# Performance work log

Hardware: AMD Instinct MI355X
Metric: run time of the kernel (lower is better)

## Reference

```python
import jax, jax.numpy as jnp
import numpy as np
from jax import lax

EPS = 1e-07
PATCH = 3  # patch_size -> padding = 1 with 1x1 kernels
PROP = 3   # propagate_size -> 3x3 sum pool (avg_pool*9)


def setup_inputs() -> dict:
    key = jax.random.key(0)
    k1, k2 = jax.random.split(key)
    foreground = jax.random.normal(k1, (4, 128, 64, 64), dtype=jnp.float32)
    mask = jax.random.uniform(k2, (4, 1, 64, 64), dtype=jnp.float32)
    return {"foreground": foreground, "mask": mask}


def _cattention_single(x, m):
    # x: (c, h, w); m: (1, h, w)
    c, h, w = x.shape
    pad = PATCH // 2  # = 1
    # dynamic 1x1 conv kernels: (h*w, c), one kernel per spatial location
    k = x.reshape(c, h * w).T + EPS
    k = k / jnp.sqrt(jnp.sum(k * k, axis=1, keepdims=True))
    # F.conv2d(x, k, padding=1) with 1x1 kernels -> zero-pad then matmul
    x_pad = jnp.pad(x, ((0, 0), (pad, pad), (pad, pad)))  # (c, h+2, w+2)
    scores = jnp.einsum('lc,cij->lij', k, x_pad)  # (hw, h+2, w+2)
    # avg_pool2d(3,1,padding=1) * 9 == 3x3 sum pool with zero padding
    scores = lax.reduce_window(scores, 0.0, lax.add,
                               window_dimensions=(1, 3, 3),
                               window_strides=(1, 1, 1),
                               padding=((0, 0), (1, 1), (1, 1)))
    att = jax.nn.softmax(scores, axis=0)  # softmax over the hw channel dim
    # conv_transpose2d with 1x1 kernels, padding=1 -> crop border then matmul
    att_c = att[:, pad:-pad, pad:-pad]  # (hw, h, w)
    recovered = jnp.einsum('lij,lc->cij', att_c, k)  # (c, h, w)
    recovered = recovered * (1.0 - m) / float(PATCH ** 2)
    return recovered + x * m


def reference(foreground, mask):
    return jax.vmap(_cattention_single)(foreground, mask)
```

## Files before the change

kernel.cpp:

```cpp
#include <hip/hip_runtime.h>


typedef short bf16x8 __attribute__((ext_vector_type(8)));
typedef float f32x4 __attribute__((ext_vector_type(4)));

#define L2E 1.4426950408889634f

__device__ __forceinline__ unsigned short f2bf(float f) {
    unsigned int u;
    __builtin_memcpy(&u, &f, 4);
    u = u + 0x7FFFu + ((u >> 16) & 1u);
    return (unsigned short)(u >> 16);
}

__global__ void prep_k(const float* __restrict__ x,
                       unsigned short* __restrict__ kmat,
                       unsigned short* __restrict__ kT) {
    const int b = blockIdx.y, l0 = blockIdx.x * 64, t = threadIdx.x;
    const int wave = t >> 6, lane = t & 63;
    const float* xb = x + (size_t)b * 128 * 4096;
    __shared__ float sqp[256];
    __shared__ __align__(16) unsigned short sT[64 * 136];

    float xv[32];
    float sq = 0.f;
#pragma unroll
    for (int i = 0; i < 32; i++) {
        int c = wave * 32 + i;
        float v = xb[(size_t)c * 4096 + l0 + lane] + 1e-7f;
        xv[i] = v;
        sq += v * v;
    }
    sqp[t] = sq;
    __syncthreads();
    const float inv = rsqrtf(sqp[lane] + sqp[64 + lane] + sqp[128 + lane] + sqp[192 + lane]);

    unsigned int* sT32 = (unsigned int*)sT;
#pragma unroll
    for (int i = 0; i < 16; i++) {
        int c = wave * 32 + i * 2;
        unsigned int pack = (unsigned int)f2bf(xv[2 * i] * inv) |
                            ((unsigned int)f2bf(xv[2 * i + 1] * inv) << 16);
        sT32[(lane * 136 + c) >> 1] = pack;
    }
    __syncthreads();
#pragma unroll
    for (int i = 0; i < 4; i++) {
        int e = i * 2048 + t * 8, row = e >> 7, col = e & 127;
        *(bf16x8*)(kmat + ((size_t)b * 4096 + l0 + row) * 128 + col) =
            *(const bf16x8*)(sT + row * 136 + col);
    }
    unsigned short* ktb = kT + (size_t)b * 128 * 4096;
#pragma unroll
    for (int i = 0; i < 32; i++) {
        int c = wave * 32 + i;
        ktb[(size_t)c * 4096 + l0 + lane] = sT[lane * 136 + c];
    }
}

__global__ void prep_xb(const float* __restrict__ x,
                        unsigned short* __restrict__ xbT) {
    const int b = blockIdx.y, p = blockIdx.x, t = threadIdx.x;
    __shared__ float sX[8][3][66];
    __shared__ __align__(16) unsigned short sQ[64 * 136];

    for (int c0 = 0; c0 < 128; c0 += 8) {
        __syncthreads();
#pragma unroll
        for (int i = 0; i < 6; i++) {
            int j = t + i * 256;
            int cc = j / 192, rem = j % 192;
            int r = rem >> 6, q = rem & 63;
            int pp = p + r - 1;
            float v = 0.f;
            if ((unsigned)pp < 64u)
                v = x[((size_t)b * 128 + c0 + cc) * 4096 + pp * 64 + q];
            sX[cc][r][1 + q] = v;
        }
        if (t < 48) {
            int cc = t / 6, r = (t % 6) >> 1, side = t & 1;
            sX[cc][r][side * 65] = 0.f;
        }
        __syncthreads();
#pragma unroll
        for (int h = 0; h < 2; h++) {
            int idx = t + h * 256;
            int cc = idx >> 6, q = idx & 63;
            float s = 0.f;
#pragma unroll
            for (int r = 0; r < 3; r++)
                s += sX[cc][r][q] + sX[cc][r][q + 1] + sX[cc][r][q + 2];
            sQ[q * 136 + c0 + cc] = f2bf(s * L2E);
        }
    }
    __syncthreads();
#pragma unroll
    for (int i = 0; i < 4; i++) {
        int e = i * 2048 + t * 8, row = e >> 7, col = e & 127;
        *(bf16x8*)(xbT + ((size_t)b * 4096 + p * 64 + row) * 128 + col) =
            *(const bf16x8*)(sQ + row * 136 + col);
    }
}

#define SK_STRIDE 136
#define SV_STRIDE 72
#define SP_STRIDE 72
#define SK_ELEMS (64 * SK_STRIDE)
#define SV_ELEMS (128 * SV_STRIDE)
#define SP_ELEMS (4 * 32 * SP_STRIDE)
#define SMEM_ELEMS (SK_ELEMS + SV_ELEMS + SP_ELEMS)

__global__ void __launch_bounds__(256, 2) flash_attn(
        const unsigned short* __restrict__ kmat,
        const unsigned short* __restrict__ kT,
        const unsigned short* __restrict__ xbT,
        float* __restrict__ opart,
        float* __restrict__ lsum,
        int nsplit) {
    const int combo = blockIdx.x & (4 * nsplit - 1);
    const int qb = blockIdx.x / (4 * nsplit);
    const int b = combo & 3, split = combo >> 2;
    const int nk = 4096 / nsplit, kt_base = split * nk, NIT = nk >> 6;
    const int t = threadIdx.x;
    const int wave = t >> 6, lane = t & 63;
    const int l16 = lane & 15, quad = lane >> 4;

    __shared__ __align__(16) unsigned short smem[SMEM_ELEMS];
    unsigned short* sK = smem;
    unsigned short* sV = smem + SK_ELEMS;
    unsigned short* sP = smem + SK_ELEMS + SV_ELEMS + wave * 32 * SP_STRIDE;

    bf16x8 aq[2][4];
#pragma unroll
    for (int h = 0; h < 2; h++) {
        const unsigned short* xq =
            xbT + ((size_t)b * 4096 + qb * 128 + wave * 32 + h * 16 + l16) * 128 + quad * 8;
#pragma unroll
        for (int cc = 0; cc < 4; cc++) aq[h][cc] = *(const bf16x8*)(xq + cc * 32);
    }

    f32x4 o[2][8];
#pragma unroll
    for (int h = 0; h < 2; h++)
#pragma unroll
        for (int n = 0; n < 8; n++) o[h][n] = (f32x4){0.f, 0.f, 0.f, 0.f};
    float rs[2][4] = {{0.f, 0.f, 0.f, 0.f}, {0.f, 0.f, 0.f, 0.f}};

    const unsigned short* kmb = kmat + (size_t)b * 4096 * 128;
    const unsigned short* ktb = kT + (size_t)b * 128 * 4096;

    bf16x8 kreg[4], vreg[4];
#pragma unroll
    for (int i = 0; i < 4; i++) {
        int e = i * 2048 + t * 8;
        kreg[i] = *(const bf16x8*)(kmb + (size_t)(kt_base + (e >> 7)) * 128 + (e & 127));
        vreg[i] = *(const bf16x8*)(ktb + (size_t)(e >> 6) * 4096 + kt_base + (e & 63));
    }

    for (int it = 0; it < NIT; it++) {
        __syncthreads();
#pragma unroll
        for (int i = 0; i < 4; i++) {
            int e = i * 2048 + t * 8;
            *(bf16x8*)(sK + (e >> 7) * SK_STRIDE + (e & 127)) = kreg[i];
            *(bf16x8*)(sV + (e >> 6) * SV_STRIDE + (e & 63)) = vreg[i];
        }
        __syncthreads();
        if (it + 1 < NIT) {
            const int kt0 = kt_base + (it + 1) * 64;
#pragma unroll
            for (int i = 0; i < 4; i++) {
                int e = i * 2048 + t * 8;
                kreg[i] = *(const bf16x8*)(kmb + (size_t)(kt0 + (e >> 7)) * 128 + (e & 127));
                vreg[i] = *(const bf16x8*)(ktb + (size_t)(e >> 6) * 4096 + kt0 + (e & 63));
            }
        }

        f32x4 s[2][4];
#pragma unroll
        for (int h = 0; h < 2; h++)
#pragma unroll
            for (int k4 = 0; k4 < 4; k4++) s[h][k4] = (f32x4){0.f, 0.f, 0.f, 0.f};
#pragma unroll
        for (int cc = 0; cc < 4; cc++) {
#pragma unroll
            for (int k4 = 0; k4 < 4; k4++) {
                bf16x8 bf = *(const bf16x8*)(sK + (k4 * 16 + l16) * SK_STRIDE + cc * 32 + quad * 8);
#pragma unroll
                for (int h = 0; h < 2; h++)
                    s[h][k4] = __builtin_amdgcn_mfma_f32_16x16x32_bf16(aq[h][cc], bf, s[h][k4], 0, 0, 0);
            }
        }

#pragma unroll
        for (int h = 0; h < 2; h++)
#pragma unroll
            for (int k4 = 0; k4 < 4; k4++)
#pragma unroll
                for (int r = 0; r < 4; r++) {
                    float p = exp2f(s[h][k4][r]);
                    s[h][k4][r] = p;
                    rs[h][r] += p;
                }

#pragma unroll
        for (int h = 0; h < 2; h++)
#pragma unroll
            for (int k4 = 0; k4 < 4; k4++)
#pragma unroll
                for (int r = 0; r < 4; r++)
                    sP[(h * 16 + quad * 4 + r) * SP_STRIDE + k4 * 16 + l16] = f2bf(s[h][k4][r]);
        asm volatile("" ::: "memory");
        __threadfence_block();
        bf16x8 pa[2][2];
#pragma unroll
        for (int h = 0; h < 2; h++)
#pragma unroll
            for (int kc = 0; kc < 2; kc++)
                pa[h][kc] = *(const bf16x8*)(sP + (h * 16 + l16) * SP_STRIDE + kc * 32 + quad * 8);
        asm volatile("" ::: "memory");

#pragma unroll
        for (int kc = 0; kc < 2; kc++)
#pragma unroll
            for (int n = 0; n < 8; n++) {
                bf16x8 bf = *(const bf16x8*)(sV + (n * 16 + l16) * SV_STRIDE + kc * 32 + quad * 8);
#pragma unroll
                for (int h = 0; h < 2; h++)
                    o[h][n] = __builtin_amdgcn_mfma_f32_16x16x32_bf16(pa[h][kc], bf, o[h][n], 0, 0, 0);
            }
    }

#pragma unroll
    for (int off = 1; off < 16; off <<= 1)
#pragma unroll
        for (int h = 0; h < 2; h++)
#pragma unroll
            for (int r = 0; r < 4; r++) rs[h][r] += __shfl_xor(rs[h][r], off);
    if (l16 == 0) {
#pragma unroll
        for (int h = 0; h < 2; h++)
#pragma unroll
            for (int r = 0; r < 4; r++) {
                int q = qb * 128 + wave * 32 + h * 16 + quad * 4 + r;
                lsum[(size_t)(split * 4 + b) * 4096 + q] = rs[h][r];
            }
    }

    float* sO = reinterpret_cast<float*>(smem);
#pragma unroll
    for (int half = 0; half < 2; half++) {
        __syncthreads();
        if ((wave >> 1) == half) {
#pragma unroll
            for (int h = 0; h < 2; h++)
#pragma unroll
                for (int n = 0; n < 8; n++)
#pragma unroll
                    for (int r = 0; r < 4; r++)
                        sO[(n * 16 + l16) * 68 + (wave & 1) * 32 + h * 16 + quad * 4 + r] =
                            o[h][n][r];
        }
        __syncthreads();
#pragma unroll
        for (int i = 0; i < 8; i++) {
            int c = (t >> 4) + i * 16, qj = (t & 15) * 4;
            *(f32x4*)(opart + ((size_t)(split * 4 + b) * 128 + c) * 4096 +
                      qb * 128 + half * 64 + qj) = *(const f32x4*)(sO + c * 68 + qj);
        }
    }
}

__global__ void combine(const float* __restrict__ opart,
                        const float* __restrict__ lsum,
                        const float* __restrict__ x,
                        const float* __restrict__ mask,
                        float* __restrict__ out, int S) {
    const int b = blockIdx.y, qb = blockIdx.x, t = threadIdx.x;
    __shared__ float Linv[64];
    if (t < 64) {
        int q = qb * 64 + t;
        float L = 0.f;
        for (int s = 0; s < S; s++) L += lsum[(size_t)(s * 4 + b) * 4096 + q];
        Linv[t] = 1.f / fmaxf(L, 1e-37f);
    }
    __syncthreads();
#pragma unroll
    for (int i = 0; i < 8; i++) {
        int c = (t >> 4) + i * 16, qj = (t & 15) * 4;
        size_t qoff = (size_t)qb * 64 + qj;
        f32x4 acc = (f32x4){0.f, 0.f, 0.f, 0.f};
        for (int s = 0; s < S; s++) {
            f32x4 p = *(const f32x4*)(opart + ((size_t)(s * 4 + b) * 128 + c) * 4096 + qoff);
#pragma unroll
            for (int j = 0; j < 4; j++) acc[j] += p[j];
        }
        f32x4 xv = *(const f32x4*)(x + ((size_t)b * 128 + c) * 4096 + qoff);
        f32x4 mv = *(const f32x4*)(mask + (size_t)b * 4096 + qoff);
        f32x4 res;
#pragma unroll
        for (int j = 0; j < 4; j++)
            res[j] = acc[j] * Linv[qj + j] * (1.f - mv[j]) * (1.f / 9.f) + xv[j] * mv[j];
        *(f32x4*)(out + ((size_t)b * 128 + c) * 4096 + qoff) = res;
    }
}

extern "C" void kernel_launch(void* const* d_in, const int* in_sizes, int n_in,
                              void* d_out, int out_size, void* d_ws, size_t ws_size,
                              hipStream_t stream) {
    const float* x = (const float*)d_in[0];
    const float* mask = (const float*)d_in[1];
    float* out = (float*)d_out;
    char* ws = (char*)d_ws;
    unsigned short* kmat = (unsigned short*)(ws);
    unsigned short* kT   = (unsigned short*)(ws + (size_t)4 * 1024 * 1024);
    unsigned short* xbT  = (unsigned short*)(ws + (size_t)8 * 1024 * 1024);
    float* lsum  = (float*)(ws + (size_t)12 * 1024 * 1024);
    float* opart = (float*)(ws + (size_t)12 * 1024 * 1024 + 512 * 1024);

    int S;
    if (ws_size >= (size_t)46661632) S = 4;
    else if (ws_size >= (size_t)29884416) S = 2;
    else if (ws_size >= (size_t)21495808) S = 1;
    else return;

    prep_k<<<dim3(64, 4), 256, 0, stream>>>(x, kmat, kT);
    prep_xb<<<dim3(64, 4), 256, 0, stream>>>(x, xbT);
    flash_attn<<<dim3(32 * 4 * S), 256, 0, stream>>>(kmat, kT, xbT, opart, lsum, S);
    combine<<<dim3(64, 4), 256, 0, stream>>>(opart, lsum, x, mask, out, S);
}
```

Measured before the change: 168.3 us.

## Fuse prep kernels, fold combine into attention via atomic last-block reduction

Merges the two prep kernels into one that computes normalized K, K transpose and the box-summed query in a single pass over x. The attention kernel now reads K fragments straight from global memory instead of staging them in LDS, stores partial outputs as bf16, and doubles the key split count with higher occupancy. The separate combine kernel is removed: the last split block per tile, detected with an atomic counter, does the reduction, normalization and mask blend. This cuts launches and traffic, but adds bf16 rounding of the partial outputs and a dependence on correct counter reset and memory fences.

```diff
diff --git a/kernel.cpp b/kernel.cpp
--- a/kernel.cpp
+++ b/kernel.cpp
@@ -3,6 +3,8 @@
 
 typedef short bf16x8 __attribute__((ext_vector_type(8)));
 typedef float f32x4 __attribute__((ext_vector_type(4)));
+typedef unsigned short u16x4 __attribute__((ext_vector_type(4)));
+typedef unsigned int u32x2 __attribute__((ext_vector_type(2)));
 
 #define L2E 1.4426950408889634f
 
@@ -12,123 +14,133 @@
     u = u + 0x7FFFu + ((u >> 16) & 1u);
     return (unsigned short)(u >> 16);
 }
-
-__global__ void prep_k(const float* __restrict__ x,
-                       unsigned short* __restrict__ kmat,
-                       unsigned short* __restrict__ kT) {
-    const int b = blockIdx.y, l0 = blockIdx.x * 64, t = threadIdx.x;
-    const int wave = t >> 6, lane = t & 63;
-    const float* xb = x + (size_t)b * 128 * 4096;
+__device__ __forceinline__ float bf2f(unsigned short h) {
+    unsigned int u = ((unsigned int)h) << 16;
+    float f;
+    __builtin_memcpy(&f, &u, 4);
+    return f;
+}
+__device__ __forceinline__ unsigned int pk_bf16(float a, float b) {
+    unsigned int ua, ub;
+    __builtin_memcpy(&ua, &a, 4);
+    __builtin_memcpy(&ub, &b, 4);
+    return ((ua + 0x8000u) >> 16) | ((ub + 0x8000u) & 0xFFFF0000u);
+}
+
+__global__ void prep(const float* __restrict__ x,
+                     unsigned short* __restrict__ kmat,
+                     unsigned short* __restrict__ kT,
+                     unsigned short* __restrict__ xbT,
+                     unsigned int* __restrict__ counters) {
+    const int p = blockIdx.x, qh = blockIdx.y, b = blockIdx.z, t = threadIdx.x;
+    const int q0 = qh * 32;
+    if (qh == 0 && t == 0) counters[b * 32 + (p >> 1)] = 0;
+
+    __shared__ float sX[8][3][36];
+    __shared__ float sMidT[32 * 132];
+    __shared__ __align__(16) unsigned short sQ[32 * 136];
     __shared__ float sqp[256];
-    __shared__ __align__(16) unsigned short sT[64 * 136];
-
-    float xv[32];
-    float sq = 0.f;
-#pragma unroll
-    for (int i = 0; i < 32; i++) {
-        int c = wave * 32 + i;
-        float v = xb[(size_t)c * 4096 + l0 + lane] + 1e-7f;
-        xv[i] = v;
-        sq += v * v;
-    }
-    sqp[t] = sq;
+    __shared__ float sInv[32];
+
+    const int ccOwn = t >> 5, qOwn = t & 31;
+    float sqacc = 0.f;
+
+    for (int c0 = 0; c0 < 128; c0 += 8) {
+        __syncthreads();
+#pragma unroll
+        for (int i = 0; i < 4; i++) {
+            int j = i * 256 + t;
+            if (j < 816) {
+                int cc = j / 102, rem = j - cc * 102;
+                int r = rem / 34, qq = rem - r * 34;
+                int pp = p + r - 1, qg = q0 + qq - 1;
+                float v = 0.f;
+                if ((unsigned)pp < 64u && (unsigned)qg < 64u)
+                    v = x[((size_t)b * 128 + c0 + cc) * 4096 + pp * 64 + qg];
+                sX[cc][r][qq] = v;
+            }
+        }
+        __syncthreads();
+        float mid = sX[ccOwn][1][qOwn + 1] + 1e-7f;
+        sMidT[qOwn * 132 + c0 + ccOwn] = mid;
+        sqacc += mid * mid;
+        float sbox = 0.f;
+#pragma unroll
+        for (int r = 0; r < 3; r++)
+            sbox += sX[ccOwn][r][qOwn] + sX[ccOwn][r][qOwn + 1] + sX[ccOwn][r][qOwn + 2];
+        sQ[qOwn * 136 + c0 + ccOwn] = f2bf(sbox * L2E);
+    }
+    sqp[ccOwn * 32 + qOwn] = sqacc;
     __syncthreads();
-    const float inv = rsqrtf(sqp[lane] + sqp[64 + lane] + sqp[128 + lane] + sqp[192 + lane]);
-
-    unsigned int* sT32 = (unsigned int*)sT;
-#pragma unroll
-    for (int i = 0; i < 16; i++) {
-        int c = wave * 32 + i * 2;
-        unsigned int pack = (unsigned int)f2bf(xv[2 * i] * inv) |
-                            ((unsigned int)f2bf(xv[2 * i + 1] * inv) << 16);
-        sT32[(lane * 136 + c) >> 1] = pack;
+    if (t < 32) {
+        float ss = 0.f;
+#pragma unroll
+        for (int g = 0; g < 8; g++) ss += sqp[g * 32 + t];
+        sInv[t] = rsqrtf(ss);
     }
     __syncthreads();
-#pragma unroll
-    for (int i = 0; i < 4; i++) {
-        int e = i * 2048 + t * 8, row = e >> 7, col = e & 127;
-        *(bf16x8*)(kmat + ((size_t)b * 4096 + l0 + row) * 128 + col) =
-            *(const bf16x8*)(sT + row * 136 + col);
-    }
-    unsigned short* ktb = kT + (size_t)b * 128 * 4096;
-#pragma unroll
-    for (int i = 0; i < 32; i++) {
-        int c = wave * 32 + i;
-        ktb[(size_t)c * 4096 + l0 + lane] = sT[lane * 136 + c];
-    }
-}
-
-__global__ void prep_xb(const float* __restrict__ x,
-                        unsigned short* __restrict__ xbT) {
-    const int b = blockIdx.y, p = blockIdx.x, t = threadIdx.x;
-    __shared__ float sX[8][3][66];
-    __shared__ __align__(16) unsigned short sQ[64 * 136];
-
-    for (int c0 = 0; c0 < 128; c0 += 8) {
-        __syncthreads();
-#pragma unroll
-        for (int i = 0; i < 6; i++) {
-            int j = t + i * 256;
-            int cc = j / 192, rem = j % 192;
-            int r = rem >> 6, q = rem & 63;
-            int pp = p + r - 1;
-            float v = 0.f;
-            if ((unsigned)pp < 64u)
-                v = x[((size_t)b * 128 + c0 + cc) * 4096 + pp * 64 + q];
-            sX[cc][r][1 + q] = v;
-        }
-        if (t < 48) {
-            int cc = t / 6, r = (t % 6) >> 1, side = t & 1;
-            sX[cc][r][side * 65] = 0.f;
-        }
-        __syncthreads();
-#pragma unroll
-        for (int h = 0; h < 2; h++) {
-            int idx = t + h * 256;
-            int cc = idx >> 6, q = idx & 63;
-            float s = 0.f;
-#pragma unroll
-            for (int r = 0; r < 3; r++)
-                s += sX[cc][r][q] + sX[cc][r][q + 1] + sX[cc][r][q + 2];
-            sQ[q * 136 + c0 + cc] = f2bf(s * L2E);
-        }
-    }
-    __syncthreads();
-#pragma unroll
-    for (int i = 0; i < 4; i++) {
-        int e = i * 2048 + t * 8, row = e >> 7, col = e & 127;
-        *(bf16x8*)(xbT + ((size_t)b * 4096 + p * 64 + row) * 128 + col) =
+
+#pragma unroll
+    for (int i = 0; i < 2; i++) {
+        int e = (i * 256 + t) * 8, row = e >> 7, col = e & 127;
+        *(bf16x8*)(xbT + ((size_t)b * 4096 + p * 64 + q0 + row) * 128 + col) =
             *(const bf16x8*)(sQ + row * 136 + col);
     }
-}
-
-#define SK_STRIDE 136
+#pragma unroll
+    for (int i = 0; i < 2; i++) {
+        int u = i * 256 + t, q = u >> 4, cg = u & 15;
+        float iv = sInv[q];
+        f32x4 a = *(const f32x4*)(sMidT + q * 132 + cg * 8);
+        f32x4 c = *(const f32x4*)(sMidT + q * 132 + cg * 8 + 4);
+        unsigned int w[4];
+        w[0] = pk_bf16(a[0] * iv, a[1] * iv);
+        w[1] = pk_bf16(a[2] * iv, a[3] * iv);
+        w[2] = pk_bf16(c[0] * iv, c[1] * iv);
+        w[3] = pk_bf16(c[2] * iv, c[3] * iv);
+        *(uint4*)(kmat + ((size_t)b * 4096 + p * 64 + q0 + q) * 128 + cg * 8) =
+            make_uint4(w[0], w[1], w[2], w[3]);
+    }
+    {
+        int c = t >> 1, half = t & 1;
+        unsigned int w[8];
+#pragma unroll
+        for (int j = 0; j < 8; j++) {
+            int ql = half * 16 + j * 2;
+            w[j] = pk_bf16(sMidT[ql * 132 + c] * sInv[ql],
+                           sMidT[(ql + 1) * 132 + c] * sInv[ql + 1]);
+        }
+        unsigned short* dst = kT + ((size_t)b * 128 + c) * 4096 + p * 64 + q0 + half * 16;
+        *(uint4*)(dst) = make_uint4(w[0], w[1], w[2], w[3]);
+        *(uint4*)(dst + 8) = make_uint4(w[4], w[5], w[6], w[7]);
+    }
+}
+
 #define SV_STRIDE 72
-#define SP_STRIDE 72
-#define SK_ELEMS (64 * SK_STRIDE)
-#define SV_ELEMS (128 * SV_STRIDE)
-#define SP_ELEMS (4 * 32 * SP_STRIDE)
-#define SMEM_ELEMS (SK_ELEMS + SV_ELEMS + SP_ELEMS)
-
-__global__ void __launch_bounds__(256, 2) flash_attn(
+
+__global__ void __launch_bounds__(256, 3) flash_attn(
         const unsigned short* __restrict__ kmat,
         const unsigned short* __restrict__ kT,
         const unsigned short* __restrict__ xbT,
-        float* __restrict__ opart,
+        const float* __restrict__ x,
+        const float* __restrict__ mask,
+        unsigned short* __restrict__ opart,
         float* __restrict__ lsum,
-        int nsplit) {
+        float* __restrict__ out,
+        unsigned int* __restrict__ counters,
+        int nsplit, int qbshift) {
     const int combo = blockIdx.x & (4 * nsplit - 1);
-    const int qb = blockIdx.x / (4 * nsplit);
+    const int qb = blockIdx.x >> qbshift;
     const int b = combo & 3, split = combo >> 2;
-    const int nk = 4096 / nsplit, kt_base = split * nk, NIT = nk >> 6;
+    const int nk = 4096 / nsplit, NIT = nk >> 6, kt_base = split * nk;
     const int t = threadIdx.x;
     const int wave = t >> 6, lane = t & 63;
     const int l16 = lane & 15, quad = lane >> 4;
 
-    __shared__ __align__(16) unsigned short smem[SMEM_ELEMS];
-    unsigned short* sK = smem;
-    unsigned short* sV = smem + SK_ELEMS;
-    unsigned short* sP = smem + SK_ELEMS + SV_ELEMS + wave * 32 * SP_STRIDE;
+    __shared__ __align__(16) unsigned short smem[18432];
+    unsigned short* sV = smem;
+    unsigned short* sP = smem + 9216 + wave * 2304;
+    __shared__ float Linv[128];
+    __shared__ int isLast;
 
     bf16x8 aq[2][4];
 #pragma unroll
@@ -144,16 +156,16 @@
     for (int h = 0; h < 2; h++)
 #pragma unroll
         for (int n = 0; n < 8; n++) o[h][n] = (f32x4){0.f, 0.f, 0.f, 0.f};
-    float rs[2][4] = {{0.f, 0.f, 0.f, 0.f}, {0.f, 0.f, 0.f, 0.f}};
+    float rs[2] = {0.f, 0.f};
 
     const unsigned short* kmb = kmat + (size_t)b * 4096 * 128;
     const unsigned short* ktb = kT + (size_t)b * 128 * 4096;
-
-    bf16x8 kreg[4], vreg[4];
+    const unsigned short* kf = kmb + (size_t)(kt_base + l16) * 128 + quad * 8;
+
+    bf16x8 vreg[4];
 #pragma unroll
     for (int i = 0; i < 4; i++) {
         int e = i * 2048 + t * 8;
-        kreg[i] = *(const bf16x8*)(kmb + (size_t)(kt_base + (e >> 7)) * 128 + (e & 127));
         vreg[i] = *(const bf16x8*)(ktb + (size_t)(e >> 6) * 4096 + kt_base + (e & 63));
     }
 
@@ -162,16 +174,14 @@
 #pragma unroll
         for (int i = 0; i < 4; i++) {
             int e = i * 2048 + t * 8;
-            *(bf16x8*)(sK + (e >> 7) * SK_STRIDE + (e & 127)) = kreg[i];
             *(bf16x8*)(sV + (e >> 6) * SV_STRIDE + (e & 63)) = vreg[i];
         }
         __syncthreads();
         if (it + 1 < NIT) {
-            const int kt0 = kt_base + (it + 1) * 64;
+            int kt0 = kt_base + (it + 1) * 64;
 #pragma unroll
             for (int i = 0; i < 4; i++) {
                 int e = i * 2048 + t * 8;
-                kreg[i] = *(const bf16x8*)(kmb + (size_t)(kt0 + (e >> 7)) * 128 + (e & 127));
                 vreg[i] = *(const bf16x8*)(ktb + (size_t)(e >> 6) * 4096 + kt0 + (e & 63));
             }
         }
@@ -181,70 +191,58 @@
         for (int h = 0; h < 2; h++)
 #pragma unroll
             for (int k4 = 0; k4 < 4; k4++) s[h][k4] = (f32x4){0.f, 0.f, 0.f, 0.f};
+        const unsigned short* kfi = kf + (size_t)it * 64 * 128;
 #pragma unroll
         for (int cc = 0; cc < 4; cc++) {
 #pragma unroll
             for (int k4 = 0; k4 < 4; k4++) {
-                bf16x8 bf = *(const bf16x8*)(sK + (k4 * 16 + l16) * SK_STRIDE + cc * 32 + quad * 8);
-#pragma unroll
-                for (int h = 0; h < 2; h++)
-                    s[h][k4] = __builtin_amdgcn_mfma_f32_16x16x32_bf16(aq[h][cc], bf, s[h][k4], 0, 0, 0);
-            }
-        }
-
+                bf16x8 kfr = *(const bf16x8*)(kfi + k4 * 2048 + cc * 32);
+                s[0][k4] = __builtin_amdgcn_mfma_f32_16x16x32_bf16(kfr, aq[0][cc], s[0][k4], 0, 0, 0);
+                s[1][k4] = __builtin_amdgcn_mfma_f32_16x16x32_bf16(kfr, aq[1][cc], s[1][k4], 0, 0, 0);
+            }
+        }
+
+#pragma unroll
+        for (int h = 0; h < 2; h++) {
+#pragma unroll
+            for (int k4 = 0; k4 < 4; k4++) {
+                float p0 = exp2f(s[h][k4][0]), p1 = exp2f(s[h][k4][1]);
+                float p2 = exp2f(s[h][k4][2]), p3 = exp2f(s[h][k4][3]);
+                rs[h] += (p0 + p1) + (p2 + p3);
+                u32x2 d;
+                d[0] = pk_bf16(p0, p1);
+                d[1] = pk_bf16(p2, p3);
+                *(u32x2*)(sP + (h * 16 + l16) * 72 + k4 * 16 + quad * 4) = d;
+            }
+        }
+        asm volatile("" ::: "memory");
+        bf16x8 pa[2][2];
 #pragma unroll
         for (int h = 0; h < 2; h++)
 #pragma unroll
-            for (int k4 = 0; k4 < 4; k4++)
-#pragma unroll
-                for (int r = 0; r < 4; r++) {
-                    float p = exp2f(s[h][k4][r]);
-                    s[h][k4][r] = p;
-                    rs[h][r] += p;
-                }
-
+            for (int kc = 0; kc < 2; kc++)
+                pa[h][kc] = *(const bf16x8*)(sP + (h * 16 + l16) * 72 + kc * 32 + quad * 8);
+        asm volatile("" ::: "memory");
+
+#pragma unroll
+        for (int kc = 0; kc < 2; kc++)
+#pragma unroll
+            for (int n = 0; n < 8; n++) {
+                bf16x8 bv = *(const bf16x8*)(sV + (n * 16 + l16) * SV_STRIDE + kc * 32 + quad * 8);
+                o[0][n] = __builtin_amdgcn_mfma_f32_16x16x32_bf16(pa[0][kc], bv, o[0][n], 0, 0, 0);
+                o[1][n] = __builtin_amdgcn_mfma_f32_16x16x32_bf16(pa[1][kc], bv, o[1][n], 0, 0, 0);
+            }
+    }
+
+#pragma unroll
+    for (int h = 0; h < 2; h++) {
+        rs[h] += __shfl_xor(rs[h], 16);
+        rs[h] += __shfl_xor(rs[h], 32);
+    }
+    if (lane < 16) {
 #pragma unroll
         for (int h = 0; h < 2; h++)
-#pragma unroll
-            for (int k4 = 0; k4 < 4; k4++)
-#pragma unroll
-                for (int r = 0; r < 4; r++)
-                    sP[(h * 16 + quad * 4 + r) * SP_STRIDE + k4 * 16 + l16] = f2bf(s[h][k4][r]);
-        asm volatile("" ::: "memory");
-        __threadfence_block();
-        bf16x8 pa[2][2];
-#pragma unroll
-        for (int h = 0; h < 2; h++)
-#pragma unroll
-            for (int kc = 0; kc < 2; kc++)
-                pa[h][kc] = *(const bf16x8*)(sP + (h * 16 + l16) * SP_STRIDE + kc * 32 + quad * 8);
-        asm volatile("" ::: "memory");
-
-#pragma unroll
-        for (int kc = 0; kc < 2; kc++)
-#pragma unroll
-            for (int n = 0; n < 8; n++) {
-                bf16x8 bf = *(const bf16x8*)(sV + (n * 16 + l16) * SV_STRIDE + kc * 32 + quad * 8);
-#pragma unroll
-                for (int h = 0; h < 2; h++)
-                    o[h][n] = __builtin_amdgcn_mfma_f32_16x16x32_bf16(pa[h][kc], bf, o[h][n], 0, 0, 0);
-            }
-    }
-
-#pragma unroll
-    for (int off = 1; off < 16; off <<= 1)
-#pragma unroll
-        for (int h = 0; h < 2; h++)
-#pragma unroll
-            for (int r = 0; r < 4; r++) rs[h][r] += __shfl_xor(rs[h][r], off);
-    if (l16 == 0) {
-#pragma unroll
-        for (int h = 0; h < 2; h++)
-#pragma unroll
-            for (int r = 0; r < 4; r++) {
-                int q = qb * 128 + wave * 32 + h * 16 + quad * 4 + r;
-                lsum[(size_t)(split * 4 + b) * 4096 + q] = rs[h][r];
-            }
+            lsum[(size_t)(split * 4 + b) * 4096 + qb * 128 + wave * 32 + h * 16 + lane] = rs[h];
     }
 
     float* sO = reinterpret_cast<float*>(smem);
@@ -263,45 +261,50 @@
         }
         __syncthreads();
 #pragma unroll
-        for (int i = 0; i < 8; i++) {
-            int c = (t >> 4) + i * 16, qj = (t & 15) * 4;
-            *(f32x4*)(opart + ((size_t)(split * 4 + b) * 128 + c) * 4096 +
-                      qb * 128 + half * 64 + qj) = *(const f32x4*)(sO + c * 68 + qj);
-        }
-    }
-}
-
-__global__ void combine(const float* __restrict__ opart,
-                        const float* __restrict__ lsum,
-                        const float* __restrict__ x,
-                        const float* __restrict__ mask,
-                        float* __restrict__ out, int S) {
-    const int b = blockIdx.y, qb = blockIdx.x, t = threadIdx.x;
-    __shared__ float Linv[64];
-    if (t < 64) {
-        int q = qb * 64 + t;
+        for (int i = 0; i < 4; i++) {
+            int u = i * 256 + t, c = u >> 3, g = u & 7;
+            f32x4 v0 = *(const f32x4*)(sO + c * 68 + g * 8);
+            f32x4 v1 = *(const f32x4*)(sO + c * 68 + g * 8 + 4);
+            unsigned int w[4];
+            w[0] = pk_bf16(v0[0], v0[1]);
+            w[1] = pk_bf16(v0[2], v0[3]);
+            w[2] = pk_bf16(v1[0], v1[1]);
+            w[3] = pk_bf16(v1[2], v1[3]);
+            *(uint4*)(opart + ((size_t)(split * 4 + b) * 128 + c) * 4096 +
+                      qb * 128 + half * 64 + g * 8) = make_uint4(w[0], w[1], w[2], w[3]);
+        }
+    }
+
+    __threadfence();
+    if (t == 0)
+        isLast = (atomicAdd(&counters[b * 32 + qb], 1u) == (unsigned)(nsplit - 1));
+    __syncthreads();
+    if (!isLast) return;
+    __threadfence();
+    if (t < 128) {
         float L = 0.f;
-        for (int s = 0; s < S; s++) L += lsum[(size_t)(s * 4 + b) * 4096 + q];
+        for (int s2 = 0; s2 < nsplit; s2++)
+            L += lsum[(size_t)(s2 * 4 + b) * 4096 + qb * 128 + t];
         Linv[t] = 1.f / fmaxf(L, 1e-37f);
     }
     __syncthreads();
-#pragma unroll
-    for (int i = 0; i < 8; i++) {
-        int c = (t >> 4) + i * 16, qj = (t & 15) * 4;
-        size_t qoff = (size_t)qb * 64 + qj;
+#pragma unroll 4
+    for (int i = 0; i < 16; i++) {
+        int u = i * 256 + t, c = u >> 5, qg = u & 31, q0 = qg * 4;
         f32x4 acc = (f32x4){0.f, 0.f, 0.f, 0.f};
-        for (int s = 0; s < S; s++) {
-            f32x4 p = *(const f32x4*)(opart + ((size_t)(s * 4 + b) * 128 + c) * 4096 + qoff);
-#pragma unroll
-            for (int j = 0; j < 4; j++) acc[j] += p[j];
-        }
-        f32x4 xv = *(const f32x4*)(x + ((size_t)b * 128 + c) * 4096 + qoff);
-        f32x4 mv = *(const f32x4*)(mask + (size_t)b * 4096 + qoff);
+        for (int s2 = 0; s2 < nsplit; s2++) {
+            u16x4 pv = *(const u16x4*)(opart + ((size_t)(s2 * 4 + b) * 128 + c) * 4096 +
+                                       qb * 128 + q0);
+#pragma unroll
+            for (int j = 0; j < 4; j++) acc[j] += bf2f(pv[j]);
+        }
+        f32x4 xv = *(const f32x4*)(x + ((size_t)b * 128 + c) * 4096 + qb * 128 + q0);
+        f32x4 mv = *(const f32x4*)(mask + (size_t)b * 4096 + qb * 128 + q0);
         f32x4 res;
 #pragma unroll
         for (int j = 0; j < 4; j++)
-            res[j] = acc[j] * Linv[qj + j] * (1.f - mv[j]) * (1.f / 9.f) + xv[j] * mv[j];
-        *(f32x4*)(out + ((size_t)b * 128 + c) * 4096 + qoff) = res;
+            res[j] = acc[j] * Linv[q0 + j] * (1.f - mv[j]) * (1.f / 9.f) + xv[j] * mv[j];
+        *(f32x4*)(out + ((size_t)b * 128 + c) * 4096 + qb * 128 + q0) = res;
     }
 }
 
@@ -315,17 +318,17 @@
     unsigned short* kmat = (unsigned short*)(ws);
     unsigned short* kT   = (unsigned short*)(ws + (size_t)4 * 1024 * 1024);
     unsigned short* xbT  = (unsigned short*)(ws + (size_t)8 * 1024 * 1024);
-    float* lsum  = (float*)(ws + (size_t)12 * 1024 * 1024);
-    float* opart = (float*)(ws + (size_t)12 * 1024 * 1024 + 512 * 1024);
-
-    int S;
-    if (ws_size >= (size_t)46661632) S = 4;
-    else if (ws_size >= (size_t)29884416) S = 2;
-    else if (ws_size >= (size_t)21495808) S = 1;
+    float* lsum          = (float*)(ws + (size_t)12 * 1024 * 1024);
+    unsigned int* counters = (unsigned int*)(ws + (size_t)12 * 1024 * 1024 + 512 * 1024);
+    unsigned short* opart  = (unsigned short*)(ws + (size_t)13 * 1024 * 1024);
+
+    int S, qbshift;
+    if (ws_size >= (size_t)45 * 1024 * 1024)      { S = 8; qbshift = 5; }
+    else if (ws_size >= (size_t)29 * 1024 * 1024) { S = 4; qbshift = 4; }
+    else if (ws_size >= (size_t)21 * 1024 * 1024) { S = 2; qbshift = 3; }
     else return;
 
-    prep_k<<<dim3(64, 4), 256, 0, stream>>>(x, kmat, kT);
-    prep_xb<<<dim3(64, 4), 256, 0, stream>>>(x, xbT);
-    flash_attn<<<dim3(32 * 4 * S), 256, 0, stream>>>(kmat, kT, xbT, opart, lsum, S);
-    combine<<<dim3(64, 4), 256, 0, stream>>>(opart, lsum, x, mask, out, S);
-}
+    prep<<<dim3(64, 2, 4), 256, 0, stream>>>(x, kmat, kT, xbT, counters);
+    flash_attn<<<dim3(32 * 4 * S), 256, 0, stream>>>(kmat, kT, xbT, x, mask,
+                                                     opart, lsum, out, counters, S, qbshift);
+}
```

Result: slower. 450.5 us (+167.6%).
